# Optimization experiments

Measured on AMD Instinct MI355X. Metric: run time of the kernel, lower is better.

Reference implementation:

```python
import jax, jax.numpy as jnp
from jax import lax
import numpy as np

V, T, K, R, H, EN, L = 10000, 100, 50, 300, 200, 800, 3
B = 128
TRAIN_SIZE = 100000
DELTA = 0.005


def setup_inputs():
    key = jax.random.key(0)
    ks = jax.random.split(key, 16)
    s = 0.02
    return {
        "bows": jax.random.uniform(ks[0], (B, V), jnp.float32) * 10.0 + 1e-3,
        "times": jax.random.randint(ks[1], (B,), 0, T),
        "rnn_inp": jax.random.uniform(ks[2], (T, V), jnp.float32),
        "rho_W": jax.random.normal(ks[3], (V, R), jnp.float32) * s,
        "mu_q_alpha": jax.random.normal(ks[4], (K, T, R), jnp.float32),
        "logsigma_q_alpha": jax.random.normal(ks[5], (K, T, R), jnp.float32) * 0.1 - 2.0,
        "qtheta_W1": jax.random.normal(ks[6], (EN, V + K), jnp.float32) * s,
        "qtheta_b1": jnp.zeros((EN,), jnp.float32),
        "qtheta_W2": jax.random.normal(ks[7], (EN, EN), jnp.float32) * s,
        "qtheta_b2": jnp.zeros((EN,), jnp.float32),
        "mu_theta_W": jax.random.normal(ks[8], (K, EN), jnp.float32) * s,
        "mu_theta_b": jnp.zeros((K,), jnp.float32),
        "ls_theta_W": jax.random.normal(ks[9], (K, EN), jnp.float32) * s,
        "ls_theta_b": jnp.zeros((K,), jnp.float32),
        "eta_map_W": jax.random.normal(ks[10], (H, V), jnp.float32) * s,
        "eta_map_b": jnp.zeros((H,), jnp.float32),
        "lstm_Wih": jax.random.normal(ks[11], (L, 4 * H, H), jnp.float32) * s,
        "lstm_Whh": jax.random.normal(ks[12], (L, 4 * H, H), jnp.float32) * s,
        "lstm_bih": jnp.zeros((L, 4 * H), jnp.float32),
        "lstm_bhh": jnp.zeros((L, 4 * H), jnp.float32),
        "mu_eta_W": jax.random.normal(ks[13], (K, H + K), jnp.float32) * s,
        "mu_eta_b": jnp.zeros((K,), jnp.float32),
        "ls_eta_W": jax.random.normal(ks[14], (K, H + K), jnp.float32) * s,
        "ls_eta_b": jnp.zeros((K,), jnp.float32),
    }


def _kl(q_mu, q_ls, p_mu, p_ls):
    # KL(N(q_mu, exp(q_ls)) || N(p_mu, exp(p_ls))), logsigma == log-variance as in torch code
    return 0.5 * jnp.sum((jnp.exp(q_ls) + (q_mu - p_mu) ** 2) / (jnp.exp(p_ls) + 1e-6) - 1.0 + p_ls - q_ls, axis=-1)


def _lstm(x, Wih, Whh, bih, bhh):
    # x: [T, H]; L stacked LSTM layers (batch of 1 squeezed), torch gate order i,f,g,o
    for l in range(Wih.shape[0]):
        Wi, Wh, bi, bh = Wih[l], Whh[l], bih[l], bhh[l]
        Hd = Wh.shape[1]

        def step(carry, xt, Wi=Wi, Wh=Wh, bi=bi, bh=bh):
            h, c = carry
            g = Wi @ xt + Wh @ h + bi + bh
            i, f, gg, o = jnp.split(g, 4)
            c = jax.nn.sigmoid(f) * c + jax.nn.sigmoid(i) * jnp.tanh(gg)
            h = jax.nn.sigmoid(o) * jnp.tanh(c)
            return (h, c), h

        z = jnp.zeros((Hd,), x.dtype)
        _, x = lax.scan(step, (z, z), x)
    return x


def _forward(bows, rnn_inp, rho_W, mu_q_alpha, logsigma_q_alpha, qtheta_W1, qtheta_b1, qtheta_W2, qtheta_b2, mu_theta_W, mu_theta_b, ls_theta_W, ls_theta_b, eta_map_W, eta_map_b, lstm_Wih, lstm_Whh, lstm_bih, lstm_bhh, mu_eta_W, mu_eta_b, ls_eta_W, ls_eta_b, times):
    log_delta = jnp.log(jnp.float32(DELTA))
    # --- eta: LSTM over word-freq sequence, then sequential mu/logsigma/KL per t ---
    out = _lstm(rnn_inp @ eta_map_W.T + eta_map_b, lstm_Wih, lstm_Whh, lstm_bih, lstm_bhh)  # [T,H]
    p_ls_seq = jnp.concatenate([jnp.zeros((1,), jnp.float32), jnp.full((T - 1,), log_delta, jnp.float32)])

    def eta_step(eta_prev, xs):
        o_t, p_ls = xs
        x = jnp.concatenate([o_t, eta_prev])
        mu = mu_eta_W @ x + mu_eta_b
        ls = ls_eta_W @ x + ls_eta_b
        kl = _kl(mu, ls, eta_prev, jnp.full_like(mu, p_ls))
        return mu, (mu, kl)  # eval-mode reparameterize -> eta_t = mu

    _, (etas, kls) = lax.scan(eta_step, jnp.zeros((K,), jnp.float32), (out, p_ls_seq))
    kl_eta = kls.sum()
    # --- theta encoder ---
    nb = bows / bows.sum(1, keepdims=True)
    eta_td = etas[times]  # [B,K]
    h = jax.nn.relu(jnp.concatenate([nb, eta_td], axis=1) @ qtheta_W1.T + qtheta_b1)
    h = jax.nn.relu(h @ qtheta_W2.T + qtheta_b2)
    mu_t = h @ mu_theta_W.T + mu_theta_b
    ls_t = h @ ls_theta_W.T + ls_theta_b
    theta = jax.nn.softmax(mu_t, axis=-1)  # z = mu (eval-mode reparam)
    coeff = jnp.float32(TRAIN_SIZE / bows.shape[0])
    kl_theta = _kl(mu_t, ls_t, eta_td, jnp.zeros_like(mu_t)).sum() * coeff
    # --- alpha: with eval-mode reparam, alphas == mu, so KL is fully vectorized ---
    muT = jnp.transpose(mu_q_alpha, (1, 0, 2))  # [T,K,R]
    lsT = jnp.transpose(logsigma_q_alpha, (1, 0, 2))
    alphas = muT
    p_mu = jnp.concatenate([jnp.zeros((1, K, R), muT.dtype), alphas[:-1]], axis=0)
    p_ls = jnp.concatenate([jnp.zeros((1, K, R), muT.dtype), jnp.full((T - 1, K, R), log_delta, muT.dtype)], axis=0)
    kl_alpha = _kl(muT, lsT, p_mu, p_ls).sum()
    # --- beta and NLL ---
    logit = alphas.reshape(T * K, R) @ rho_W.T  # [T*K, V]
    beta = jax.nn.softmax(logit, axis=-1).reshape(T, K, V)
    beta_d = beta[times]  # [B,K,V]
    loglik = jnp.log(jnp.einsum('bk,bkv->bv', theta, beta_d) + 1e-12)
    nll = (-(loglik * bows).sum(-1)).sum() * coeff
    loss = nll + kl_eta + kl_theta + kl_alpha
    return loss, nll, kl_eta, kl_theta, kl_alpha


def reference(bows, times, rnn_inp, rho_W, mu_q_alpha, logsigma_q_alpha, qtheta_W1, qtheta_b1, qtheta_W2, qtheta_b2, mu_theta_W, mu_theta_b, ls_theta_W, ls_theta_b, eta_map_W, eta_map_b, lstm_Wih, lstm_Whh, lstm_bih, lstm_bhh, mu_eta_W, mu_eta_b, ls_eta_W, ls_eta_b):
    return _forward(bows, rnn_inp, rho_W, mu_q_alpha, logsigma_q_alpha, qtheta_W1, qtheta_b1, qtheta_W2, qtheta_b2, mu_theta_W, mu_theta_b, ls_theta_W, ls_theta_b, eta_map_W, eta_map_b, lstm_Wih, lstm_Whh, lstm_bih, lstm_bhh, mu_eta_W, mu_eta_b, ls_eta_W, ls_eta_b, times)
```

## Files before the change

kernel.cpp:

```cpp
#include <hip/hip_runtime.h>


typedef unsigned int u32;
typedef unsigned short u16;
typedef _Float16 f16;
typedef f16 f16x2 __attribute__((ext_vector_type(2)));
typedef short bf16x8 __attribute__((ext_vector_type(8)));
typedef float f32x4 __attribute__((ext_vector_type(4)));
typedef u32 u32x4 __attribute__((ext_vector_type(4)));

#define LOG_DELTA (-5.2983174f)
#define COEFF 781.25f

#if defined(__has_builtin)
#if __has_builtin(__builtin_amdgcn_sdot4)
#define HAVE_SDOT4 1
#endif
#endif

__device__ __forceinline__ float bf2f(u16 a) { return __uint_as_float(((u32)a) << 16); }
__device__ __forceinline__ u16 f2bf(float f) {
  u32 u = __float_as_uint(f);
  u32 r = (u + 0x7fffu + ((u >> 16) & 1u)) >> 16;
  return (u16)r;
}
__device__ __forceinline__ int dot4i8(u32 a, u32 b, int c) {
#ifdef HAVE_SDOT4
  return __builtin_amdgcn_sdot4(a, b, c, false);
#else
  int s = c;
  s += ((int)(a << 24) >> 24) * ((int)(b << 24) >> 24);
  s += ((int)(a << 16) >> 24) * ((int)(b << 16) >> 24);
  s += ((int)(a << 8) >> 24) * ((int)(b << 8) >> 24);
  s += ((int)a >> 24) * ((int)b >> 24);
  return s;
#endif
}
__device__ __forceinline__ float sigm(float x) { return 1.f / (1.f + __expf(-x)); }
__device__ __forceinline__ float ftanh(float x) { float t = __expf(2.f * x); return (t - 1.f) / (t + 1.f); }
__device__ __forceinline__ u16 f2h(float x) { return __builtin_bit_cast(u16, (f16)x); }
__device__ __forceinline__ float h2f(u16 x) { return (float)__builtin_bit_cast(f16, x); }
__device__ __forceinline__ void async_load16(const u16* g, u16* l) {
  __builtin_amdgcn_global_load_lds((const __attribute__((address_space(1))) u32*)g,
                                   (__attribute__((address_space(3))) u32*)l, 16, 0, 0);
}


__global__ __launch_bounds__(64) void k_zero(float* __restrict__ accum) {
  if (threadIdx.x < 8) accum[threadIdx.x] = 0.f;
}

__global__ __launch_bounds__(256) void k_nb(const float* __restrict__ bows, float* __restrict__ nb) {
  __shared__ float red[256];
  const int b = blockIdx.x, tid = threadIdx.x;
  float s = 0.f;
  for (int v = tid; v < 10000; v += 256) s += bows[b * 10000 + v];
  red[tid] = s; __syncthreads();
  for (int o = 128; o > 0; o >>= 1) { if (tid < o) red[tid] += red[tid + o]; __syncthreads(); }
  const float inv = 1.f / red[0];
  for (int v = tid; v < 10000; v += 256) nb[b * 10000 + v] = bows[b * 10000 + v] * inv;
}

__global__ __launch_bounds__(256) void k_bsum(const float* __restrict__ a, const float* __restrict__ b,
                                              float* __restrict__ o, int n) {
  int i = blockIdx.x * 256 + threadIdx.x;
  if (i < n) o[i] = a[i] + b[i];
}

__global__ __launch_bounds__(256) void k_fill(float* __restrict__ C, const float* __restrict__ bias,
                                              int N, int total) {
  for (int i = blockIdx.x * 256 + threadIdx.x; i < total; i += gridDim.x * 256)
    C[i] = bias[i % N];
}

__global__ __launch_bounds__(128) void k_stack2(const float* __restrict__ a, const float* __restrict__ b,
                                                float* __restrict__ o) {
  const int t = threadIdx.x;
  if (t < 50) o[t] = a[t];
  else if (t < 100) o[t] = b[t - 50];
}

template<int EPI>
__global__ __launch_bounds__(256) void k_reduceZ(const float* __restrict__ P,
                                                 const float* __restrict__ bias,
                                                 float* __restrict__ out,
                                                 int N, int total, int Z) {
  for (int i = blockIdx.x * 256 + threadIdx.x; i < total; i += gridDim.x * 256) {
    float s = bias[i % N];
    for (int z = 0; z < Z; ++z) s += P[(size_t)z * total + i];
    if (EPI == 2) s = s > 0.f ? s : 0.f;
    out[i] = s;
  }
}

__global__ __launch_bounds__(64) void k_quant_whh(const float* __restrict__ Whh,
                                                  u32* __restrict__ whq, float* __restrict__ rowscale) {
  const int gr = blockIdx.x;
  const int lane = threadIdx.x;
  __shared__ float wrow[200];
  const float* src = Whh + (size_t)gr * 200;
  float m = 0.f;
  for (int c = lane; c < 200; c += 64) { float v = src[c]; wrow[c] = v; m = fmaxf(m, fabsf(v)); }
  for (int o = 32; o > 0; o >>= 1) m = fmaxf(m, __shfl_down(m, o));
  m = __shfl(m, 0);
  const float qs = (m > 0.f) ? 127.f / m : 0.f;
  __syncthreads();
  const int l = gr / 800, rr = gr - l * 800;
  if (lane < 52) {
    u32 d = 0;
    if (lane < 50) {
#pragma unroll
      for (int b = 0; b < 4; ++b) {
        int q = __float2int_rn(wrow[lane * 4 + b] * qs);
        q = max(-127, min(127, q));
        d |= ((u32)(q & 0xff)) << (8 * b);
      }
    }
    whq[l * 41600 + rr * 52 + lane] = d;
  }
  if (lane == 0) rowscale[gr] = (m > 0.f) ? m / 127.f : 0.f;
}

__global__ __launch_bounds__(256) void k_prep_A(const float* __restrict__ muq, u16* __restrict__ Abf) {
  int idx = blockIdx.x * 256 + threadIdx.x;
  if (idx >= 5120 * 320) return;
  int r = idx % 320, m = idx / 320;
  float v = 0.f;
  if (r < 300 && m < 5000) { int t = m / 50, k = m - t * 50; v = muq[k * 30000 + t * 300 + r]; }
  Abf[idx] = f2bf(v);
}
__global__ __launch_bounds__(256) void k_prep_B(const float* __restrict__ rho, u16* __restrict__ Bbf) {
  int idx = blockIdx.x * 256 + threadIdx.x;
  if (idx >= 10112 * 320) return;
  int r = idx % 320, n = idx / 320;
  float v = (r < 300 && n < 10000) ? rho[n * 300 + r] : 0.f;
  Bbf[idx] = f2bf(v);
}


#define ST 64
#define SBK 32

template<int AMODE, int BMODE, int EPI>
__global__ __launch_bounds__(256) void gemm64(
    const float* __restrict__ A, const float* __restrict__ Bm, const float* __restrict__ Bm2,
    const float* __restrict__ bias, float* __restrict__ C,
    int M, int N, int Kd, int lda, int ldb,
    const int* __restrict__ times, const float* __restrict__ etas)
{
  __shared__ __align__(16) float As[SBK][ST + 4];
  __shared__ __align__(16) float Bs[SBK][ST + 4];
  const int tid = threadIdx.x;
  const int tx = tid & 15, ty = tid >> 4;
  const int m_base = blockIdx.x * ST, n_base = blockIdx.y * ST;
  float acc[4][4] = {};
  const int nkt = (Kd + SBK - 1) / SBK;
  const int per = (nkt + gridDim.z - 1) / gridDim.z;
  const int kt0 = blockIdx.z * per;
  const int kt1 = min(nkt, kt0 + per);
  const int lkk = tid & 31;
  const int lrow = tid >> 5;
  for (int kt = kt0; kt < kt1; ++kt) {
    const int kg = kt * SBK + lkk;
#pragma unroll
    for (int i = 0; i < 8; ++i) {
      const int m = m_base + lrow + i * 8;
      float v = 0.f;
      if (m < M && kg < Kd) {
        if (AMODE == 0) v = A[(size_t)m * lda + kg];
        else {
          if (kg < 10000) v = A[(size_t)m * 10000 + kg];
          else v = etas[times[m] * 50 + (kg - 10000)];
        }
      }
      As[lkk][lrow + i * 8] = v;
    }
#pragma unroll
    for (int i = 0; i < 8; ++i) {
      const int n = n_base + lrow + i * 8;
      float v = 0.f;
      if (n < N && kg < Kd) {
        if (BMODE == 0) v = Bm[(size_t)n * ldb + kg];
        else v = (n < 50) ? Bm[(size_t)n * ldb + kg] : Bm2[(size_t)(n - 50) * ldb + kg];
      }
      Bs[lkk][lrow + i * 8] = v;
    }
    __syncthreads();
#pragma unroll
    for (int kk = 0; kk < SBK; ++kk) {
      const float4 a4 = *(const float4*)&As[kk][ty * 4];
      const float4 b4 = *(const float4*)&Bs[kk][tx * 4];
      const float av[4] = {a4.x, a4.y, a4.z, a4.w};
      const float bv[4] = {b4.x, b4.y, b4.z, b4.w};
#pragma unroll
      for (int i = 0; i < 4; ++i)
#pragma unroll
        for (int j = 0; j < 4; ++j) acc[i][j] += av[i] * bv[j];
    }
    __syncthreads();
  }
#pragma unroll
  for (int i = 0; i < 4; ++i) {
    const int m = m_base + ty * 4 + i;
    if (m >= M) continue;
#pragma unroll
    for (int j = 0; j < 4; ++j) {
      const int n = n_base + tx * 4 + j;
      if (n >= N) continue;
      float v = acc[i][j];
      if (EPI == 1) { C[(size_t)m * N + n] = v + bias[n]; }
      else if (EPI == 2) { v += bias[n]; C[(size_t)m * N + n] = v > 0.f ? v : 0.f; }
      else if (EPI == 5) { atomicAdd(&C[(size_t)m * N + n], v); }
      else { C[(size_t)m * N + n] = v; }
    }
  }
}


#define LT 128
#define LBK 32

template<int AMODE>
__global__ __launch_bounds__(256) void gemm128p(
    const float* __restrict__ A, const float* __restrict__ Bm,
    float* __restrict__ P,
    int M, int N, int Kd, int lda, int ldb,
    const int* __restrict__ times, const float* __restrict__ etas)
{
  __shared__ __align__(16) float As[LBK][LT + 4];
  __shared__ __align__(16) float Bs[LBK][LT + 4];
  const int tid = threadIdx.x;
  const int tx = tid & 15, ty = tid >> 4;
  const int m_base = blockIdx.x * LT, n_base = blockIdx.y * LT;
  const int nkt = (Kd + LBK - 1) / LBK;
  const int per = (nkt + gridDim.z - 1) / gridDim.z;
  const int kt0 = blockIdx.z * per;
  const int kt1 = min(nkt, kt0 + per);
  const int lkk = tid & 31;
  const int lrow = tid >> 5;
  float acc[8][8] = {};
  float pa[16], pb[16];
  {
    const int kg = kt0 * LBK + lkk;
#pragma unroll
    for (int i = 0; i < 16; ++i) {
      const int m = m_base + lrow + i * 8;
      float v = 0.f;
      if (m < M && kg < Kd) {
        if (AMODE == 0) v = A[(size_t)m * lda + kg];
        else v = (kg < 10000) ? A[(size_t)m * 10000 + kg] : etas[times[m] * 50 + (kg - 10000)];
      }
      pa[i] = v;
      const int n = n_base + lrow + i * 8;
      float w = 0.f;
      if (n < N && kg < Kd) w = Bm[(size_t)n * ldb + kg];
      pb[i] = w;
    }
  }
  for (int kt = kt0; kt < kt1; ++kt) {
#pragma unroll
    for (int i = 0; i < 16; ++i) {
      As[lkk][lrow + i * 8] = pa[i];
      Bs[lkk][lrow + i * 8] = pb[i];
    }
    __syncthreads();
    if (kt + 1 < kt1) {
      const int kg = (kt + 1) * LBK + lkk;
#pragma unroll
      for (int i = 0; i < 16; ++i) {
        const int m = m_base + lrow + i * 8;
        float v = 0.f;
        if (m < M && kg < Kd) {
          if (AMODE == 0) v = A[(size_t)m * lda + kg];
          else v = (kg < 10000) ? A[(size_t)m * 10000 + kg] : etas[times[m] * 50 + (kg - 10000)];
        }
        pa[i] = v;
        const int n = n_base + lrow + i * 8;
        float w = 0.f;
        if (n < N && kg < Kd) w = Bm[(size_t)n * ldb + kg];
        pb[i] = w;
      }
    }
#pragma unroll
    for (int kk = 0; kk < LBK; ++kk) {
      const float4* ap = (const float4*)&As[kk][ty * 8];
      const float4* bp = (const float4*)&Bs[kk][tx * 8];
      const float4 a0 = ap[0], a1 = ap[1];
      const float4 b0 = bp[0], b1 = bp[1];
      const float av[8] = {a0.x, a0.y, a0.z, a0.w, a1.x, a1.y, a1.z, a1.w};
      const float bv[8] = {b0.x, b0.y, b0.z, b0.w, b1.x, b1.y, b1.z, b1.w};
#pragma unroll
      for (int i = 0; i < 8; ++i)
#pragma unroll
        for (int j = 0; j < 8; ++j) acc[i][j] += av[i] * bv[j];
    }
    __syncthreads();
  }
  float* Cz = P + (size_t)blockIdx.z * M * N;
#pragma unroll
  for (int i = 0; i < 8; ++i) {
    const int m = m_base + ty * 8 + i;
    if (m >= M) continue;
#pragma unroll
    for (int j = 0; j < 8; ++j) {
      const int n = n_base + tx * 8 + j;
      if (n >= N) continue;
      Cz[(size_t)m * N + n] = acc[i][j];
    }
  }
}


__global__ __launch_bounds__(256) void gemm_mfma_bT(
    const u16* __restrict__ A, const u16* __restrict__ B, u16* __restrict__ C,
    int M, int N)
{
  __shared__ u16 As[128 * 32];
  __shared__ u16 Bs[128 * 32];
  const int tid = threadIdx.x;
  const int l = tid & 63, w = tid >> 6;
  const int wm = w & 1, wn = w >> 1;
  const int m0 = blockIdx.x * 128, n0 = blockIdx.y * 128;
  f32x4 acc[4][4] = {};
  const int arow = l >> 2;
  const int acol = (l & 3) * 8;
  for (int kt = 0; kt < 10; ++kt) {
    const int k0 = kt * 32;
#pragma unroll
    for (int c = 0; c < 2; ++c) {
      const int i = w + c * 4;
      async_load16(A + (size_t)(m0 + i * 16 + arow) * 320 + k0 + acol, As + i * 512);
      async_load16(B + (size_t)(n0 + i * 16 + arow) * 320 + k0 + acol, Bs + i * 512);
    }
    __syncthreads();
    bf16x8 af[4], bfr[4];
#pragma unroll
    for (int x = 0; x < 4; ++x) {
      af[x]  = *(const bf16x8*)&As[(wm * 64 + x * 16 + (l & 15)) * 32 + (l >> 4) * 8];
      bfr[x] = *(const bf16x8*)&Bs[(wn * 64 + x * 16 + (l & 15)) * 32 + (l >> 4) * 8];
    }
#pragma unroll
    for (int x = 0; x < 4; ++x)
#pragma unroll
      for (int y = 0; y < 4; ++y)
        acc[x][y] = __builtin_amdgcn_mfma_f32_16x16x32_bf16(af[x], bfr[y], acc[x][y], 0, 0, 0);
    __syncthreads();
  }
  const int col = l & 15, quad = l >> 4;
#pragma unroll
  for (int x = 0; x < 4; ++x) {
    const int gmB = m0 + wm * 64 + x * 16 + quad * 4;
#pragma unroll
    for (int y = 0; y < 4; ++y) {
      const int gn = n0 + wn * 64 + y * 16 + col;
      if (gn >= N) continue;
#pragma unroll
      for (int r = 0; r < 4; ++r) {
        const int gm = gmB + r;
        if (gm < M) C[(size_t)gm * N + gn] = f2bf(acc[x][y][r]);
      }
    }
  }
}


__global__ __launch_bounds__(512, 1) void lstm_scan_reg(
    const u32* __restrict__ whq,
    const float* __restrict__ rowscale,
    const float* __restrict__ xproj,
    float* __restrict__ hseq)
{
  __shared__ u16 pg[800];
  __shared__ __align__(16) u32 hq[52];
  __shared__ float wmax[8];
  __shared__ float hscale_s[1];
  const int tid = threadIdx.x;
  const int act = (tid < 400);
  const int rA = act ? tid : 399;
  const int rB = rA + 400;
  u32x4 wA4[13], wB4[13];
  {
    const u32x4* gA = (const u32x4*)(whq + (size_t)rA * 52);
    const u32x4* gB = (const u32x4*)(whq + (size_t)rB * 52);
#pragma unroll
    for (int i = 0; i < 13; ++i) { wA4[i] = gA[i]; wB4[i] = gB[i]; }
  }
#pragma unroll
  for (int i = 0; i < 13; ++i)
    asm volatile("" : "+v"(wA4[i]), "+v"(wB4[i]));
  float rsA = 0.f, rsB = 0.f;
  float xpA = 0.f, xpB = 0.f;
  if (act) {
    rsA = rowscale[tid]; rsB = rowscale[tid + 400];
    xpA = xproj[tid]; xpB = xproj[tid + 400];
  }
  if (tid < 52) hq[tid] = 0;
  if (tid < 8) wmax[tid] = 0.f;
  if (tid == 0) hscale_s[0] = 0.f;
  float c_reg = 0.f;
  __syncthreads();
  for (int t = 0; t < 100; ++t) {
    if (act) {
      float nxA = 0.f, nxB = 0.f;
      if (t < 99) { nxA = xproj[(t + 1) * 800 + tid]; nxB = xproj[(t + 1) * 800 + tid + 400]; }
      const float hdq = hscale_s[0];
      u32x4 hv4[13];
#pragma unroll
      for (int i = 0; i < 13; ++i) hv4[i] = *((const u32x4*)hq + i);
      int aA = 0, aB = 0;
#pragma unroll
      for (int g = 0; g < 50; ++g) {
        const u32 h = hv4[g >> 2][g & 3];
        aA = dot4i8(wA4[g >> 2][g & 3], h, aA);
        aB = dot4i8(wB4[g >> 2][g & 3], h, aB);
      }
      pg[tid] = f2h((float)aA * (rsA * hdq) + xpA);
      pg[tid + 400] = f2h((float)aB * (rsB * hdq) + xpB);
      xpA = nxA; xpB = nxB;
    }
    __syncthreads();
    float hv = 0.f;
    if (tid < 200) {
      float gi = sigm(h2f(pg[tid]));
      float gf = sigm(h2f(pg[200 + tid]));
      float gg = ftanh(h2f(pg[400 + tid]));
      float go = sigm(h2f(pg[600 + tid]));
      c_reg = gf * c_reg + gi * gg;
      hv = go * ftanh(c_reg);
      hseq[t * 200 + tid] = hv;
    }
    float m = fabsf(hv);
    for (int o = 32; o > 0; o >>= 1) m = fmaxf(m, __shfl_down(m, o));
    if ((tid & 63) == 0) wmax[tid >> 6] = m;
    __syncthreads();
    if (tid < 200) {
      const float hm = fmaxf(fmaxf(wmax[0], wmax[1]), fmaxf(wmax[2], wmax[3]));
      const float qs = (hm > 0.f) ? 127.f / hm : 0.f;
      int q = __float2int_rn(hv * qs);
      q = max(-127, min(127, q));
      ((signed char*)hq)[tid] = (signed char)q;
      if (tid == 0) hscale_s[0] = (hm > 0.f) ? hm / 127.f : 0.f;
    }
    __syncthreads();
  }
}


__global__ __launch_bounds__(64, 1) void eta_scan_reg(
    const float* __restrict__ muW, const float* __restrict__ lsW,
    const float* __restrict__ pc0,
    float* __restrict__ etas, float* __restrict__ accum)
{
  __shared__ __align__(16) float ep[52];
  const int j = threadIdx.x;
  const int act = (j < 50);
  float wmu[52], wls[52];
  if (act) {
#pragma unroll
    for (int k = 0; k < 25; ++k) {
      float2 a = *(const float2*)(muW + (size_t)j * 250 + 200 + 2 * k);
      float2 b = *(const float2*)(lsW + (size_t)j * 250 + 200 + 2 * k);
      wmu[2 * k] = a.x; wmu[2 * k + 1] = a.y;
      wls[2 * k] = b.x; wls[2 * k + 1] = b.y;
    }
    wmu[50] = wmu[51] = wls[50] = wls[51] = 0.f;
  } else {
#pragma unroll
    for (int k = 0; k < 52; ++k) { wmu[k] = 0.f; wls[k] = 0.f; }
  }
  if (j < 52) ep[j] = 0.f;
  float klacc = 0.f;
  float mye = 0.f;
  float pmu = act ? pc0[j] : 0.f;
  float pls_ = act ? pc0[50 + j] : 0.f;
  __syncthreads();
  for (int t = 0; t < 100; ++t) {
    float nmu = 0.f, nls = 0.f;
    if (act && t < 99) { nmu = pc0[(t + 1) * 100 + j]; nls = pc0[(t + 1) * 100 + 50 + j]; }
    float ma[4] = {pmu, 0.f, 0.f, 0.f};
    float la[4] = {pls_, 0.f, 0.f, 0.f};
    const float4* e4 = (const float4*)ep;
#pragma unroll
    for (int i = 0; i < 13; ++i) {
      const float4 e = e4[i];
      ma[0] += wmu[4 * i + 0] * e.x; ma[1] += wmu[4 * i + 1] * e.y;
      ma[2] += wmu[4 * i + 2] * e.z; ma[3] += wmu[4 * i + 3] * e.w;
      la[0] += wls[4 * i + 0] * e.x; la[1] += wls[4 * i + 1] * e.y;
      la[2] += wls[4 * i + 2] * e.z; la[3] += wls[4 * i + 3] * e.w;
    }
    const float mu = (ma[0] + ma[1]) + (ma[2] + ma[3]);
    const float ls = (la[0] + la[1]) + (la[2] + la[3]);
    __syncthreads();
    if (act) {
      const float pls = (t == 0) ? 0.f : LOG_DELTA;
      const float pv = __expf(pls) + 1e-6f;
      const float d = mu - mye;
      klacc += 0.5f * ((__expf(ls) + d * d) / pv - 1.f + pls - ls);
      etas[t * 50 + j] = mu;
      mye = mu;
      ep[j] = mu;
    }
    __syncthreads();
    pmu = nmu; pls_ = nls;
  }
  for (int o = 32; o > 0; o >>= 1) klacc += __shfl_down(klacc, o);
  if (j == 0) accum[0] = klacc;
}


__global__ __launch_bounds__(64) void k_theta(const float* __restrict__ mul,
                                              const float* __restrict__ etas, const int* __restrict__ times,
                                              float* __restrict__ theta, float* __restrict__ accum) {
  const int b = blockIdx.x, lane = threadIdx.x;
  float m_ = 0.f, l_ = 0.f, e_ = 0.f, mx = -1e30f;
  if (lane < 50) {
    m_ = mul[b * 100 + lane];
    l_ = mul[b * 100 + 50 + lane];
    e_ = etas[times[b] * 50 + lane];
    mx = m_;
  }
  for (int o = 32; o > 0; o >>= 1) mx = fmaxf(mx, __shfl_down(mx, o));
  mx = __shfl(mx, 0);
  float ex = (lane < 50) ? __expf(m_ - mx) : 0.f;
  float sum = ex;
  for (int o = 32; o > 0; o >>= 1) sum += __shfl_down(sum, o);
  sum = __shfl(sum, 0);
  if (lane < 50) theta[b * 50 + lane] = ex / sum;
  float kl = 0.f;
  if (lane < 50) {
    float d = m_ - e_;
    kl = 0.5f * ((__expf(l_) + d * d) / (1.f + 1e-6f) - 1.f - l_);
  }
  for (int o = 32; o > 0; o >>= 1) kl += __shfl_down(kl, o);
  if (lane == 0) atomicAdd(accum + 1, kl);
}


__global__ __launch_bounds__(256) void k_rowsum(const u16* __restrict__ logit, float* __restrict__ Z) {
  const int r = blockIdx.x, tid = threadIdx.x;
  const u32* row = (const u32*)(logit + (size_t)r * 10000);
  __shared__ float red[256];
  float s = 0.f;
  for (int v = tid; v < 5000; v += 256) {
    u32 p = row[v];
    s += __expf(bf2f((u16)(p & 0xffffu))) + __expf(bf2f((u16)(p >> 16)));
  }
  red[tid] = s; __syncthreads();
  for (int o = 128; o > 0; o >>= 1) { if (tid < o) red[tid] += red[tid + o]; __syncthreads(); }
  if (tid == 0) Z[r] = red[0];
}


__global__ __launch_bounds__(256) void k_nll(const u16* __restrict__ logit, const float* __restrict__ Z,
                                             const float* __restrict__ theta, const float* __restrict__ bows,
                                             const int* __restrict__ times, float* __restrict__ accum) {
  const int b = blockIdx.x, seg = blockIdx.y, tid = threadIdx.x;
  const int t = times[b];
  __shared__ float c2[52];
  __shared__ float red[256];
  if (tid < 50) c2[tid] = theta[b * 50 + tid] / Z[t * 50 + tid];
  __syncthreads();
  float part = 0.f;
  const int v0 = seg * 1250, v1 = v0 + 1250;
  const u16* base = logit + (size_t)t * 500000;
  for (int v = v0 + tid; v < v1; v += 256) {
    float ssv = 1e-12f;
#pragma unroll
    for (int k = 0; k < 50; ++k) ssv += c2[k] * __expf(bf2f(base[k * 10000 + v]));
    part += bows[b * 10000 + v] * __logf(ssv);
  }
  red[tid] = part; __syncthreads();
  for (int o = 128; o > 0; o >>= 1) { if (tid < o) red[tid] += red[tid + o]; __syncthreads(); }
  if (tid == 0) atomicAdd(accum + 3, -red[0]);
}


__global__ __launch_bounds__(256) void k_alpha_kl(const float* __restrict__ muq, const float* __restrict__ lsq,
                                                  float* __restrict__ accum) {
  __shared__ float red[256];
  const int tid = threadIdx.x;
  float s = 0.f;
  for (int i = blockIdx.x * 256 + tid; i < 1500000; i += gridDim.x * 256) {
    int r = i % 300;
    int tk = i / 300;
    int k = tk % 50;
    int t = tk / 50;
    size_t idx = (size_t)k * 30000 + (size_t)t * 300 + r;
    float mu = muq[idx], ls = lsq[idx];
    float pm = 0.f, pls = 0.f;
    if (t > 0) { pm = muq[idx - 300]; pls = LOG_DELTA; }
    float d = mu - pm;
    s += 0.5f * ((__expf(ls) + d * d) / (__expf(pls) + 1e-6f) - 1.f + pls - ls);
  }
  red[tid] = s; __syncthreads();
  for (int o = 128; o > 0; o >>= 1) { if (tid < o) red[tid] += red[tid + o]; __syncthreads(); }
  if (tid == 0) atomicAdd(accum + 2, red[0]);
}


__global__ __launch_bounds__(64) void k_final(const float* __restrict__ accum, float* __restrict__ out) {
  if (threadIdx.x == 0) {
    float nll = accum[3] * COEFF;
    float kl_eta = accum[0];
    float kl_theta = accum[1] * COEFF;
    float kl_alpha = accum[2];
    out[0] = nll + kl_eta + kl_theta + kl_alpha;
    out[1] = nll;
    out[2] = kl_eta;
    out[3] = kl_theta;
    out[4] = kl_alpha;
  }
}


extern "C" void kernel_launch(void* const* d_in, const int* in_sizes, int n_in,
                              void* d_out, int out_size, void* d_ws, size_t ws_size,
                              hipStream_t stream) {
  (void)in_sizes; (void)n_in; (void)out_size; (void)ws_size;
  const float* bows   = (const float*)d_in[0];
  const int*   times  = (const int*)d_in[1];
  const float* rnn_in = (const float*)d_in[2];
  const float* rho_W  = (const float*)d_in[3];
  const float* muq    = (const float*)d_in[4];
  const float* lsq    = (const float*)d_in[5];
  const float* qW1    = (const float*)d_in[6];
  const float* qb1    = (const float*)d_in[7];
  const float* qW2    = (const float*)d_in[8];
  const float* qb2    = (const float*)d_in[9];
  const float* muthW  = (const float*)d_in[10];
  const float* muthb  = (const float*)d_in[11];
  const float* lsthW  = (const float*)d_in[12];
  const float* lsthb  = (const float*)d_in[13];
  const float* emW    = (const float*)d_in[14];
  const float* emb    = (const float*)d_in[15];
  const float* Wih    = (const float*)d_in[16];
  const float* Whh    = (const float*)d_in[17];
  const float* bih    = (const float*)d_in[18];
  const float* bhh    = (const float*)d_in[19];
  const float* mueW   = (const float*)d_in[20];
  const float* mueb   = (const float*)d_in[21];
  const float* lseW   = (const float*)d_in[22];
  const float* lseb   = (const float*)d_in[23];
  float* out = (float*)d_out;
  float* ws = (float*)d_ws;

  float* accum = ws + 0;
  float* nb    = ws + 8;
  float* x0    = ws + 1280008;
  float* xproj = ws + 1300008;
  float* hsA   = ws + 1380008;
  float* hsB   = ws + 1400008;
  u32*   whq   = (u32*)(ws + 1420008);
  float* rowsc = ws + 1544808;
  float* bias2 = ws + 1547208;
  float* pc0   = ws + 1547408;
  float* bias2e= ws + 1558008;
  float* hsC   = ws + 1560008;
  float* bsum  = ws + 1660008;
  float* etas  = ws + 1662408;
  float* h1    = ws + 1667408;
  float* h2    = ws + 1769808;
  float* mul   = ws + 1872208;
  float* theta = ws + 1885008;
  float* Zrow  = ws + 1891408;
  u16*   A_bf  = (u16*)(ws + 1896408);
  u16*   B_bf  = (u16*)(ws + 2715608);
  u16*   logit = (u16*)(ws + 4333528);
  float* P1    = ws + 4333528;
  float* Px0   = ws + 8941528;
  float* P2    = ws + 10221528;

  k_zero<<<1, 64, 0, stream>>>(accum);
  k_nb<<<128, 256, 0, stream>>>(bows, nb);
  k_quant_whh<<<2400, 64, 0, stream>>>(Whh, whq, rowsc);
  k_bsum<<<10, 256, 0, stream>>>(bih, bhh, bsum, 2400);
  k_prep_A<<<6400, 256, 0, stream>>>(muq, A_bf);
  k_prep_B<<<12640, 256, 0, stream>>>(rho_W, B_bf);
  k_stack2<<<1, 128, 0, stream>>>(muthb, lsthb, bias2);
  k_stack2<<<1, 128, 0, stream>>>(mueb, lseb, bias2e);
  k_fill<<<40, 256, 0, stream>>>(pc0, bias2e, 100, 10000);

  gemm128p<0><<<dim3(1, 2, 64), 256, 0, stream>>>(rnn_in, emW, Px0,
                                                  100, 200, 10000, 10000, 10000, nullptr, nullptr);
  k_reduceZ<1><<<79, 256, 0, stream>>>(Px0, emb, x0, 200, 20000, 64);

  const float* lin[3] = {x0, hsA, hsB};
  float* lout[3] = {hsA, hsB, hsC};
  for (int l = 0; l < 3; ++l) {
    gemm64<0, 0, 1><<<dim3(2, 13, 1), 256, 0, stream>>>(lin[l], Wih + l * 160000, nullptr,
                                                        bsum + l * 800, xproj,
                                                        100, 800, 200, 200, 200, nullptr, nullptr);
    lstm_scan_reg<<<1, 512, 0, stream>>>(whq + l * 41600, rowsc + l * 800, xproj, lout[l]);
  }
  gemm64<0, 1, 5><<<dim3(2, 2, 7), 256, 0, stream>>>(hsC, mueW, lseW, nullptr, pc0,
                                                     100, 100, 200, 200, 250, nullptr, nullptr);
  eta_scan_reg<<<1, 64, 0, stream>>>(mueW, lseW, pc0, etas, accum);

  gemm128p<2><<<dim3(1, 7, 45), 256, 0, stream>>>(nb, qW1, P1,
                                                  128, 800, 10050, 10000, 10050, times, etas);
  k_reduceZ<2><<<400, 256, 0, stream>>>(P1, qb1, h1, 800, 102400, 45);
  gemm128p<0><<<dim3(1, 7, 5), 256, 0, stream>>>(h1, qW2, P2,
                                                 128, 800, 800, 800, 800, nullptr, nullptr);
  k_reduceZ<2><<<400, 256, 0, stream>>>(P2, qb2, h2, 800, 102400, 5);
  k_fill<<<50, 256, 0, stream>>>(mul, bias2, 100, 12800);
  gemm64<0, 1, 5><<<dim3(2, 2, 5), 256, 0, stream>>>(h2, muthW, lsthW, nullptr, mul,
                                                     128, 100, 800, 800, 800, nullptr, nullptr);
  k_theta<<<128, 64, 0, stream>>>(mul, etas, times, theta, accum);

  gemm_mfma_bT<<<dim3(40, 79), 256, 0, stream>>>(A_bf, B_bf, logit, 5000, 10000);
  k_rowsum<<<5000, 256, 0, stream>>>(logit, Zrow);
  k_nll<<<dim3(128, 8), 256, 0, stream>>>(logit, Zrow, theta, bows, times, accum);

  k_alpha_kl<<<512, 256, 0, stream>>>(muq, lsq, accum);
  k_final<<<1, 64, 0, stream>>>(accum, out);
}
```

Baseline: 1.109 ms.

## Fuse prep kernels and chain LSTM layers in one persistent kernel with grid barriers

```diff
diff --git a/kernel.cpp b/kernel.cpp
--- a/kernel.cpp
+++ b/kernel.cpp
@@ -45,73 +45,92 @@
                                    (__attribute__((address_space(3))) u32*)l, 16, 0, 0);
 }
 
-
-__global__ __launch_bounds__(64) void k_zero(float* __restrict__ accum) {
-  if (threadIdx.x < 8) accum[threadIdx.x] = 0.f;
-}
-
-__global__ __launch_bounds__(256) void k_nb(const float* __restrict__ bows, float* __restrict__ nb) {
-  __shared__ float red[256];
-  const int b = blockIdx.x, tid = threadIdx.x;
-  float s = 0.f;
-  for (int v = tid; v < 10000; v += 256) s += bows[b * 10000 + v];
-  red[tid] = s; __syncthreads();
-  for (int o = 128; o > 0; o >>= 1) { if (tid < o) red[tid] += red[tid + o]; __syncthreads(); }
-  const float inv = 1.f / red[0];
-  for (int v = tid; v < 10000; v += 256) nb[b * 10000 + v] = bows[b * 10000 + v] * inv;
-}
-
-__global__ __launch_bounds__(256) void k_bsum(const float* __restrict__ a, const float* __restrict__ b,
-                                              float* __restrict__ o, int n) {
-  int i = blockIdx.x * 256 + threadIdx.x;
-  if (i < n) o[i] = a[i] + b[i];
-}
-
-__global__ __launch_bounds__(256) void k_fill(float* __restrict__ C, const float* __restrict__ bias,
-                                              int N, int total) {
-  for (int i = blockIdx.x * 256 + threadIdx.x; i < total; i += gridDim.x * 256)
-    C[i] = bias[i % N];
-}
-
-__global__ __launch_bounds__(128) void k_stack2(const float* __restrict__ a, const float* __restrict__ b,
-                                                float* __restrict__ o) {
-  const int t = threadIdx.x;
-  if (t < 50) o[t] = a[t];
-  else if (t < 100) o[t] = b[t - 50];
-}
-
-template<int EPI>
-__global__ __launch_bounds__(256) void k_reduceZ(const float* __restrict__ P,
-                                                 const float* __restrict__ bias,
-                                                 float* __restrict__ out,
-                                                 int N, int total, int Z) {
-  for (int i = blockIdx.x * 256 + threadIdx.x; i < total; i += gridDim.x * 256) {
-    float s = bias[i % N];
-    for (int z = 0; z < Z; ++z) s += P[(size_t)z * total + i];
-    if (EPI == 2) s = s > 0.f ? s : 0.f;
-    out[i] = s;
-  }
-}
-
-__global__ __launch_bounds__(64) void k_quant_whh(const float* __restrict__ Whh,
-                                                  u32* __restrict__ whq, float* __restrict__ rowscale) {
-  const int gr = blockIdx.x;
-  const int lane = threadIdx.x;
-  __shared__ float wrow[200];
+__device__ __forceinline__ void gbar(u32* bar, int idx, u32 target) {
+  __syncthreads();
+  __threadfence();
+  if (threadIdx.x == 0) {
+    atomicAdd(&bar[idx], 1u);
+    while (atomicAdd(&bar[idx], 0u) < target) __builtin_amdgcn_s_sleep(8);
+  }
+  __threadfence();
+  __syncthreads();
+}
+
+
+__global__ __launch_bounds__(256) void k_init(
+    const float* __restrict__ bih, const float* __restrict__ bhh, float* __restrict__ bsum,
+    const float* __restrict__ muthb, const float* __restrict__ lsthb, float* __restrict__ mul,
+    const float* __restrict__ muq, const float* __restrict__ lsq, float* __restrict__ alphapart,
+    float* __restrict__ accum, u32* __restrict__ bar) {
+  const int bx = blockIdx.x, tid = threadIdx.x;
+  if (bx < 10) {
+    int i = bx * 256 + tid;
+    if (i < 2400) bsum[i] = bih[i] + bhh[i];
+    return;
+  }
+  if (bx == 10) {
+    if (tid < 8) accum[tid] = 0.f;
+    else if (tid < 16) bar[tid - 8] = 0u;
+    return;
+  }
+  if (bx < 523) {
+    __shared__ float red[256];
+    float s = 0.f;
+    for (int i = (bx - 11) * 256 + tid; i < 1500000; i += 512 * 256) {
+      int r = i % 300;
+      int tk = i / 300;
+      int k = tk % 50;
+      int t = tk / 50;
+      size_t idx = (size_t)k * 30000 + (size_t)t * 300 + r;
+      float mu = muq[idx], ls = lsq[idx];
+      float pm = 0.f, pls = 0.f;
+      if (t > 0) { pm = muq[idx - 300]; pls = LOG_DELTA; }
+      float d = mu - pm;
+      s += 0.5f * ((__expf(ls) + d * d) / (__expf(pls) + 1e-6f) - 1.f + pls - ls);
+    }
+    red[tid] = s; __syncthreads();
+    for (int o = 128; o > 0; o >>= 1) { if (tid < o) red[tid] += red[tid + o]; __syncthreads(); }
+    if (tid == 0) alphapart[bx - 11] = red[0];
+    return;
+  }
+  {
+    int i = (bx - 523) * 256 + tid;
+    if (i < 12800) { int c = i % 100; mul[i] = (c < 50) ? muthb[c] : lsthb[c - 50]; }
+  }
+}
+
+
+__global__ __launch_bounds__(256) void k_nbquant(
+    const float* __restrict__ bows, float* __restrict__ nb,
+    const float* __restrict__ Whh, u32* __restrict__ whq, float* __restrict__ rowscale) {
+  const int tid = threadIdx.x;
+  if (blockIdx.x < 128) {
+    __shared__ float red[256];
+    const int b = blockIdx.x;
+    float s = 0.f;
+    for (int v = tid; v < 10000; v += 256) s += bows[b * 10000 + v];
+    red[tid] = s; __syncthreads();
+    for (int o = 128; o > 0; o >>= 1) { if (tid < o) red[tid] += red[tid + o]; __syncthreads(); }
+    const float inv = 1.f / red[0];
+    for (int v = tid; v < 10000; v += 256) nb[b * 10000 + v] = bows[b * 10000 + v] * inv;
+    return;
+  }
+  __shared__ float wrow[4][200];
+  const int wave = tid >> 6, lane = tid & 63;
+  const int gr = (blockIdx.x - 128) * 4 + wave;
   const float* src = Whh + (size_t)gr * 200;
   float m = 0.f;
-  for (int c = lane; c < 200; c += 64) { float v = src[c]; wrow[c] = v; m = fmaxf(m, fabsf(v)); }
+  for (int c = lane; c < 200; c += 64) { float v = src[c]; wrow[wave][c] = v; m = fmaxf(m, fabsf(v)); }
   for (int o = 32; o > 0; o >>= 1) m = fmaxf(m, __shfl_down(m, o));
   m = __shfl(m, 0);
   const float qs = (m > 0.f) ? 127.f / m : 0.f;
-  __syncthreads();
   const int l = gr / 800, rr = gr - l * 800;
   if (lane < 52) {
     u32 d = 0;
     if (lane < 50) {
 #pragma unroll
       for (int b = 0; b < 4; ++b) {
-        int q = __float2int_rn(wrow[lane * 4 + b] * qs);
+        int q = __float2int_rn(wrow[wave][lane * 4 + b] * qs);
         q = max(-127, min(127, q));
         d |= ((u32)(q & 0xff)) << (8 * b);
       }
@@ -121,16 +140,20 @@
   if (lane == 0) rowscale[gr] = (m > 0.f) ? m / 127.f : 0.f;
 }
 
-__global__ __launch_bounds__(256) void k_prep_A(const float* __restrict__ muq, u16* __restrict__ Abf) {
-  int idx = blockIdx.x * 256 + threadIdx.x;
-  if (idx >= 5120 * 320) return;
-  int r = idx % 320, m = idx / 320;
-  float v = 0.f;
-  if (r < 300 && m < 5000) { int t = m / 50, k = m - t * 50; v = muq[k * 30000 + t * 300 + r]; }
-  Abf[idx] = f2bf(v);
-}
-__global__ __launch_bounds__(256) void k_prep_B(const float* __restrict__ rho, u16* __restrict__ Bbf) {
-  int idx = blockIdx.x * 256 + threadIdx.x;
+
+__global__ __launch_bounds__(256) void k_prepAB(const float* __restrict__ muq,
+                                                const float* __restrict__ rho,
+                                                u16* __restrict__ Abf, u16* __restrict__ Bbf) {
+  if (blockIdx.x < 6400) {
+    int idx = blockIdx.x * 256 + threadIdx.x;
+    if (idx >= 5120 * 320) return;
+    int r = idx % 320, m = idx / 320;
+    float v = 0.f;
+    if (r < 300 && m < 5000) { int t = m / 50, k = m - t * 50; v = muq[k * 30000 + t * 300 + r]; }
+    Abf[idx] = f2bf(v);
+    return;
+  }
+  int idx = (blockIdx.x - 6400) * 256 + threadIdx.x;
   if (idx >= 10112 * 320) return;
   int r = idx % 320, n = idx / 320;
   float v = (r < 300 && n < 10000) ? rho[n * 300 + r] : 0.f;
@@ -310,6 +333,19 @@
   }
 }
 
+template<int EPI>
+__global__ __launch_bounds__(256) void k_reduceZ(const float* __restrict__ P,
+                                                 const float* __restrict__ bias,
+                                                 float* __restrict__ out,
+                                                 int N, int total, int Z) {
+  for (int i = blockIdx.x * 256 + threadIdx.x; i < total; i += gridDim.x * 256) {
+    float s = bias[i % N];
+    for (int z = 0; z < Z; ++z) s += P[(size_t)z * total + i];
+    if (EPI == 2) s = s > 0.f ? s : 0.f;
+    out[i] = s;
+  }
+}
+
 
 __global__ __launch_bounds__(256) void gemm_mfma_bT(
     const u16* __restrict__ A, const u16* __restrict__ B, u16* __restrict__ C,
@@ -364,12 +400,51 @@
 }
 
 
-__global__ __launch_bounds__(512, 1) void lstm_scan_reg(
-    const u32* __restrict__ whq,
-    const float* __restrict__ rowscale,
-    const float* __restrict__ xproj,
-    float* __restrict__ hseq)
-{
+#define NBLK 27
+
+__device__ void mv800(const float* __restrict__ W, const float* __restrict__ lin,
+                      const float* __restrict__ bias, float* __restrict__ outp, int bi) {
+  const int gw = bi * 8 + (threadIdx.x >> 6);
+  const int lane = threadIdx.x & 63;
+  for (int r = gw; r < 800; r += NBLK * 8) {
+    const float* Wr = W + (size_t)r * 200;
+    const float bv = bias[r];
+    for (int tt = lane; tt < 100; tt += 64) {
+      const float* xr = lin + tt * 200;
+      float a0 = 0.f, a1 = 0.f, a2 = 0.f, a3 = 0.f;
+#pragma unroll 10
+      for (int k = 0; k < 200; k += 4) {
+        a0 += Wr[k] * xr[k];     a1 += Wr[k + 1] * xr[k + 1];
+        a2 += Wr[k + 2] * xr[k + 2]; a3 += Wr[k + 3] * xr[k + 3];
+      }
+      outp[tt * 800 + r] = (a0 + a1) + (a2 + a3) + bv;
+    }
+  }
+}
+
+__device__ void mv_pc0(const float* __restrict__ muW, const float* __restrict__ lsW,
+                       const float* __restrict__ mub, const float* __restrict__ lsb,
+                       const float* __restrict__ hsC, float* __restrict__ pc0, int bi) {
+  const int gw = bi * 8 + (threadIdx.x >> 6);
+  const int lane = threadIdx.x & 63;
+  for (int j = gw; j < 100; j += NBLK * 8) {
+    const float* Wr = (j < 50) ? (muW + (size_t)j * 250) : (lsW + (size_t)(j - 50) * 250);
+    const float bv = (j < 50) ? mub[j] : lsb[j - 50];
+    for (int tt = lane; tt < 100; tt += 64) {
+      const float* xr = hsC + tt * 200;
+      float a0 = 0.f, a1 = 0.f, a2 = 0.f, a3 = 0.f;
+#pragma unroll 10
+      for (int k = 0; k < 200; k += 4) {
+        a0 += Wr[k] * xr[k];     a1 += Wr[k + 1] * xr[k + 1];
+        a2 += Wr[k + 2] * xr[k + 2]; a3 += Wr[k + 3] * xr[k + 3];
+      }
+      pc0[tt * 100 + j] = (a0 + a1) + (a2 + a3) + bv;
+    }
+  }
+}
+
+__device__ void scan_body(const u32* __restrict__ whq, const float* __restrict__ rowscale,
+                          const float* __restrict__ xproj, float* __restrict__ hseq) {
   __shared__ u16 pg[800];
   __shared__ __align__(16) u32 hq[52];
   __shared__ float wmax[8];
@@ -377,19 +452,12 @@
   const int tid = threadIdx.x;
   const int act = (tid < 400);
   const int rA = act ? tid : 399;
-  const int rB = rA + 400;
+  const u32x4* gA = (const u32x4*)(whq + (size_t)rA * 52);
+  const u32x4* gB = (const u32x4*)(whq + (size_t)(rA + 400) * 52);
   u32x4 wA4[13], wB4[13];
-  {
-    const u32x4* gA = (const u32x4*)(whq + (size_t)rA * 52);
-    const u32x4* gB = (const u32x4*)(whq + (size_t)rB * 52);
-#pragma unroll
-    for (int i = 0; i < 13; ++i) { wA4[i] = gA[i]; wB4[i] = gB[i]; }
-  }
-#pragma unroll
-  for (int i = 0; i < 13; ++i)
-    asm volatile("" : "+v"(wA4[i]), "+v"(wB4[i]));
-  float rsA = 0.f, rsB = 0.f;
-  float xpA = 0.f, xpB = 0.f;
+#pragma unroll
+  for (int i = 0; i < 13; ++i) { wA4[i] = gA[i]; wB4[i] = gB[i]; }
+  float rsA = 0.f, rsB = 0.f, xpA = 0.f, xpB = 0.f;
   if (act) {
     rsA = rowscale[tid]; rsB = rowscale[tid + 400];
     xpA = xproj[tid]; xpB = xproj[tid + 400];
@@ -445,29 +513,24 @@
   }
 }
 
-
-__global__ __launch_bounds__(64, 1) void eta_scan_reg(
-    const float* __restrict__ muW, const float* __restrict__ lsW,
-    const float* __restrict__ pc0,
-    float* __restrict__ etas, float* __restrict__ accum)
-{
+__device__ void eta_body(const float* __restrict__ muW, const float* __restrict__ lsW,
+                         const float* __restrict__ pc0, float* __restrict__ etas,
+                         float* __restrict__ accum) {
   __shared__ __align__(16) float ep[52];
   const int j = threadIdx.x;
   const int act = (j < 50);
+  const int jc = act ? j : 49;
+  const float* bm = muW + (size_t)jc * 250 + 200;
+  const float* bl = lsW + (size_t)jc * 250 + 200;
   float wmu[52], wls[52];
-  if (act) {
-#pragma unroll
-    for (int k = 0; k < 25; ++k) {
-      float2 a = *(const float2*)(muW + (size_t)j * 250 + 200 + 2 * k);
-      float2 b = *(const float2*)(lsW + (size_t)j * 250 + 200 + 2 * k);
-      wmu[2 * k] = a.x; wmu[2 * k + 1] = a.y;
-      wls[2 * k] = b.x; wls[2 * k + 1] = b.y;
-    }
-    wmu[50] = wmu[51] = wls[50] = wls[51] = 0.f;
-  } else {
-#pragma unroll
-    for (int k = 0; k < 52; ++k) { wmu[k] = 0.f; wls[k] = 0.f; }
-  }
+#pragma unroll
+  for (int k = 0; k < 25; ++k) {
+    float2 a = *(const float2*)(bm + 2 * k);
+    float2 b = *(const float2*)(bl + 2 * k);
+    wmu[2 * k] = a.x; wmu[2 * k + 1] = a.y;
+    wls[2 * k] = b.x; wls[2 * k + 1] = b.y;
+  }
+  wmu[50] = wmu[51] = wls[50] = wls[51] = 0.f;
   if (j < 52) ep[j] = 0.f;
   float klacc = 0.f;
   float mye = 0.f;
@@ -505,6 +568,30 @@
   }
   for (int o = 32; o > 0; o >>= 1) klacc += __shfl_down(klacc, o);
   if (j == 0) accum[0] = klacc;
+}
+
+__global__ __launch_bounds__(512, 1) void lstm_chain(
+    const u32* __restrict__ whq, const float* __restrict__ rowsc,
+    const float* __restrict__ Wih, const float* __restrict__ bsum,
+    const float* __restrict__ x0, float* __restrict__ xproj,
+    float* __restrict__ hsA, float* __restrict__ hsB, float* __restrict__ hsC,
+    const float* __restrict__ mueW, const float* __restrict__ lseW,
+    const float* __restrict__ mueb, const float* __restrict__ lseb,
+    float* __restrict__ pc0, float* __restrict__ etas, float* __restrict__ accum,
+    u32* __restrict__ bar)
+{
+  const int bi = blockIdx.x;
+  const float* lin[3] = {x0, hsA, hsB};
+  float* lout[3] = {hsA, hsB, hsC};
+  for (int l = 0; l < 3; ++l) {
+    mv800(Wih + (size_t)l * 160000, lin[l], bsum + l * 800, xproj, bi);
+    gbar(bar, 2 * l, NBLK);
+    if (bi == 0) scan_body(whq + (size_t)l * 41600, rowsc + l * 800, xproj, lout[l]);
+    gbar(bar, 2 * l + 1, NBLK);
+  }
+  mv_pc0(mueW, lseW, mueb, lseb, hsC, pc0, bi);
+  gbar(bar, 6, NBLK);
+  if (bi == 0) eta_body(mueW, lseW, pc0, etas, accum);
 }
 
 
@@ -575,35 +662,18 @@
 }
 
 
-__global__ __launch_bounds__(256) void k_alpha_kl(const float* __restrict__ muq, const float* __restrict__ lsq,
-                                                  float* __restrict__ accum) {
-  __shared__ float red[256];
+__global__ __launch_bounds__(64) void k_final(const float* __restrict__ accum,
+                                              const float* __restrict__ alphapart,
+                                              float* __restrict__ out) {
   const int tid = threadIdx.x;
   float s = 0.f;
-  for (int i = blockIdx.x * 256 + tid; i < 1500000; i += gridDim.x * 256) {
-    int r = i % 300;
-    int tk = i / 300;
-    int k = tk % 50;
-    int t = tk / 50;
-    size_t idx = (size_t)k * 30000 + (size_t)t * 300 + r;
-    float mu = muq[idx], ls = lsq[idx];
-    float pm = 0.f, pls = 0.f;
-    if (t > 0) { pm = muq[idx - 300]; pls = LOG_DELTA; }
-    float d = mu - pm;
-    s += 0.5f * ((__expf(ls) + d * d) / (__expf(pls) + 1e-6f) - 1.f + pls - ls);
-  }
-  red[tid] = s; __syncthreads();
-  for (int o = 128; o > 0; o >>= 1) { if (tid < o) red[tid] += red[tid + o]; __syncthreads(); }
-  if (tid == 0) atomicAdd(accum + 2, red[0]);
-}
-
-
-__global__ __launch_bounds__(64) void k_final(const float* __restrict__ accum, float* __restrict__ out) {
-  if (threadIdx.x == 0) {
+  for (int i = tid; i < 512; i += 64) s += alphapart[i];
+  for (int o = 32; o > 0; o >>= 1) s += __shfl_down(s, o);
+  if (tid == 0) {
     float nll = accum[3] * COEFF;
     float kl_eta = accum[0];
     float kl_theta = accum[1] * COEFF;
-    float kl_alpha = accum[2];
+    float kl_alpha = s;
     out[0] = nll + kl_eta + kl_theta + kl_alpha;
     out[1] = nll;
     out[2] = kl_eta;
@@ -652,9 +722,9 @@
   float* hsB   = ws + 1400008;
   u32*   whq   = (u32*)(ws + 1420008);
   float* rowsc = ws + 1544808;
-  float* bias2 = ws + 1547208;
+  u32*   bar   = (u32*)(ws + 1547208);
   float* pc0   = ws + 1547408;
-  float* bias2e= ws + 1558008;
+  float* alphp = ws + 1558008;
   float* hsC   = ws + 1560008;
   float* bsum  = ws + 1660008;
   float* etas  = ws + 1662408;
@@ -670,31 +740,18 @@
   float* Px0   = ws + 8941528;
   float* P2    = ws + 10221528;
 
-  k_zero<<<1, 64, 0, stream>>>(accum);
-  k_nb<<<128, 256, 0, stream>>>(bows, nb);
-  k_quant_whh<<<2400, 64, 0, stream>>>(Whh, whq, rowsc);
-  k_bsum<<<10, 256, 0, stream>>>(bih, bhh, bsum, 2400);
-  k_prep_A<<<6400, 256, 0, stream>>>(muq, A_bf);
-  k_prep_B<<<12640, 256, 0, stream>>>(rho_W, B_bf);
-  k_stack2<<<1, 128, 0, stream>>>(muthb, lsthb, bias2);
-  k_stack2<<<1, 128, 0, stream>>>(mueb, lseb, bias2e);
-  k_fill<<<40, 256, 0, stream>>>(pc0, bias2e, 100, 10000);
+  k_init<<<573, 256, 0, stream>>>(bih, bhh, bsum, muthb, lsthb, mul,
+                                  muq, lsq, alphp, accum, bar);
+  k_nbquant<<<728, 256, 0, stream>>>(bows, nb, Whh, whq, rowsc);
+  k_prepAB<<<19040, 256, 0, stream>>>(muq, rho_W, A_bf, B_bf);
 
   gemm128p<0><<<dim3(1, 2, 64), 256, 0, stream>>>(rnn_in, emW, Px0,
                                                   100, 200, 10000, 10000, 10000, nullptr, nullptr);
   k_reduceZ<1><<<79, 256, 0, stream>>>(Px0, emb, x0, 200, 20000, 64);
 
-  const float* lin[3] = {x0, hsA, hsB};
-  float* lout[3] = {hsA, hsB, hsC};
-  for (int l = 0; l < 3; ++l) {
-    gemm64<0, 0, 1><<<dim3(2, 13, 1), 256, 0, stream>>>(lin[l], Wih + l * 160000, nullptr,
-                                                        bsum + l * 800, xproj,
-                                                        100, 800, 200, 200, 200, nullptr, nullptr);
-    lstm_scan_reg<<<1, 512, 0, stream>>>(whq + l * 41600, rowsc + l * 800, xproj, lout[l]);
-  }
-  gemm64<0, 1, 5><<<dim3(2, 2, 7), 256, 0, stream>>>(hsC, mueW, lseW, nullptr, pc0,
-                                                     100, 100, 200, 200, 250, nullptr, nullptr);
-  eta_scan_reg<<<1, 64, 0, stream>>>(mueW, lseW, pc0, etas, accum);
+  lstm_chain<<<NBLK, 512, 0, stream>>>(whq, rowsc, Wih, bsum, x0, xproj,
+                                       hsA, hsB, hsC, mueW, lseW, mueb, lseb,
+                                       pc0, etas, accum, bar);
 
   gemm128p<2><<<dim3(1, 7, 45), 256, 0, stream>>>(nb, qW1, P1,
                                                   128, 800, 10050, 10000, 10050, times, etas);
@@ -702,7 +759,6 @@
   gemm128p<0><<<dim3(1, 7, 5), 256, 0, stream>>>(h1, qW2, P2,
                                                  128, 800, 800, 800, 800, nullptr, nullptr);
   k_reduceZ<2><<<400, 256, 0, stream>>>(P2, qb2, h2, 800, 102400, 5);
-  k_fill<<<50, 256, 0, stream>>>(mul, bias2, 100, 12800);
   gemm64<0, 1, 5><<<dim3(2, 2, 5), 256, 0, stream>>>(h2, muthW, lsthW, nullptr, mul,
                                                      128, 100, 800, 800, 800, nullptr, nullptr);
   k_theta<<<128, 64, 0, stream>>>(mul, etas, times, theta, accum);
@@ -711,6 +767,5 @@
   k_rowsum<<<5000, 256, 0, stream>>>(logit, Zrow);
   k_nll<<<dim3(128, 8), 256, 0, stream>>>(logit, Zrow, theta, bows, times, accum);
 
-  k_alpha_kl<<<512, 256, 0, stream>>>(muq, lsq, accum);
-  k_final<<<1, 64, 0, stream>>>(accum, out);
-}
+  k_final<<<1, 64, 0, stream>>>(accum, alphp, out);
+}
```

Measured after the change: 1.294 ms. 16.6% more time.
